# Optimization experiments

Measured on AMD Instinct MI355X. Metric: run time of the kernel, lower is better.

Reference implementation:

```python
import jax, jax.numpy as jnp
import numpy as np

B, S, H = 1, 2048, 4096
NH, NKV, D = 32, 8, 128
ROPE_THETA = 10000.0


def _rotate_half(x):
    half = x.shape[-1] // 2
    return jnp.concatenate([-x[..., half:], x[..., :half]], axis=-1)


def _rope_cos_sin(position_ids, dim, theta):
    inv_freq = 1.0 / (theta ** (jnp.arange(0, dim, 2, dtype=jnp.float32) / dim))  # [D/2]
    freqs = position_ids.astype(jnp.float32)[..., None] * inv_freq  # [B,S,D/2]
    emb = jnp.concatenate([freqs, freqs], axis=-1)  # [B,S,D]
    return jnp.cos(emb)[:, None], jnp.sin(emb)[:, None]  # [B,1,S,D]


def setup_inputs() -> dict:
    key = jax.random.key(0)
    k1, k2, k3 = jax.random.split(key, 3)
    hidden_states = jax.random.normal(k1, (B, S, H), dtype=jnp.float32)
    # fused QKV weight: columns = [NH*D | NKV*D | NKV*D]
    w_qkv = jax.random.normal(k2, (H, (NH + 2 * NKV) * D), dtype=jnp.float32) * (1.0 / np.sqrt(H))
    w_o = jax.random.normal(k3, (NH * D, H), dtype=jnp.float32) * (1.0 / np.sqrt(NH * D))
    attention_mask = jnp.tril(jnp.ones((S, S), dtype=bool))[None, None]  # causal [1,1,S,S]
    position_ids = jnp.arange(S, dtype=jnp.int64 if jax.config.jax_enable_x64 else jnp.int32)[None, :]
    return {"hidden_states": hidden_states, "w_qkv": w_qkv, "w_o": w_o,
            "attention_mask": attention_mask, "position_ids": position_ids}


def reference(hidden_states, w_qkv, w_o, attention_mask, position_ids):
    bsz, q_len, _ = hidden_states.shape
    qk_scale = 1.0 / np.sqrt(D)

    # fused QKV projection
    qkv = jnp.einsum('bsh,hc->bsc', hidden_states, w_qkv)
    q = qkv[..., : NH * D].reshape(bsz, q_len, NH, D).transpose(0, 2, 1, 3)        # [B,NH,S,D]
    k = qkv[..., NH * D: (NH + NKV) * D].reshape(bsz, q_len, NKV, D).transpose(0, 2, 1, 3)
    v = qkv[..., (NH + NKV) * D:].reshape(bsz, q_len, NKV, D).transpose(0, 2, 1, 3)

    # RoPE
    cos, sin = _rope_cos_sin(position_ids, D, ROPE_THETA)
    q = q * cos + _rotate_half(q) * sin
    k = k * cos + _rotate_half(k) * sin

    # GQA expand kv heads
    groups = NH // NKV
    k = jnp.repeat(k, groups, axis=1)  # [B,NH,S,D]
    v = jnp.repeat(v, groups, axis=1)

    # causal masked attention (eager path, matches scaled_qk + softmax(fp32))
    scores = jnp.einsum('bhqd,bhkd->bhqk', q, k) * qk_scale
    scores = jnp.where(attention_mask, scores, jnp.finfo(scores.dtype).min)
    probs = jax.nn.softmax(scores.astype(jnp.float32), axis=-1).astype(q.dtype)
    attn = jnp.einsum('bhqk,bhkd->bhqd', probs, v)  # [B,NH,S,D]

    # merge heads + output projection
    attn = attn.transpose(0, 2, 1, 3).reshape(bsz, q_len, NH * D)
    return jnp.einsum('bsd,dh->bsh', attn, w_o)
```

## Files before the change

### kernel.cpp

```cpp
#include <hip/hip_runtime.h>
#include <cstdint>
#include <cstddef>


#define DEV __device__ __forceinline__

typedef __attribute__((ext_vector_type(4))) float  f32x4;
typedef __attribute__((ext_vector_type(4))) short  short4v;
typedef __attribute__((ext_vector_type(8))) short  short8;
typedef __attribute__((ext_vector_type(8))) __bf16 bf16x8;

DEV short f32_to_bf16(float x) {
  union { float f; uint32_t u; } v; v.f = x;
  uint32_t r = v.u + 0x7fffu + ((v.u >> 16) & 1u);
  return (short)(r >> 16);
}

union frag_u { short4v h[2]; bf16x8 v; short s[8]; uint32_t u[4]; };
DEV bf16x8 comb(short4v lo, short4v hi) { frag_u u; u.h[0] = lo; u.h[1] = hi; return u.v; }

DEV uint32_t pack2bf_trunc(float a, float b) {
  union { float f; uint32_t u; } x, y; x.f = a; y.f = b;
  return (x.u >> 16) | (y.u & 0xFFFF0000u);
}

DEV f32x4 MFMA(bf16x8 a, bf16x8 b, f32x4 c) {
  return __builtin_amdgcn_mfma_f32_16x16x32_bf16(a, b, c, 0, 0, 0);
}

typedef __attribute__((address_space(1))) void* gas1p;
typedef __attribute__((address_space(3))) void* as3p;
DEV void gld16(const void* g, void* l) {
  __builtin_amdgcn_global_load_lds((gas1p)g, (as3p)l, 16, 0, 0);
}

#define VMCNT(n) asm volatile("s_waitcnt vmcnt(" #n ")" ::: "memory")


__global__ __launch_bounds__(256) void k_cvt_bf16(const float* __restrict__ x,
                                                  short* __restrict__ y, int n4) {
  int i = blockIdx.x * 256 + threadIdx.x;
  int stride = gridDim.x * 256;
  for (; i < n4; i += stride) {
    f32x4 v = ((const f32x4*)x)[i];
    short4v o;
    o[0] = f32_to_bf16(v[0]); o[1] = f32_to_bf16(v[1]);
    o[2] = f32_to_bf16(v[2]); o[3] = f32_to_bf16(v[3]);
    ((short4v*)y)[i] = o;
  }
}

__global__ __launch_bounds__(256) void k_transpose64(const float* __restrict__ src,
                                                     short* __restrict__ dst,
                                                     int R, int C, int stride) {
  __shared__ float tile[64][65];
  const int c0 = blockIdx.x * 64, r0 = blockIdx.y * 64;
  const int t = threadIdx.x;
  const int lr = t >> 4;
  const int lc = (t & 15) * 4;
  #pragma unroll
  for (int p = 0; p < 4; ++p) {
    const int r = p * 16 + lr;
    f32x4 v = *(const f32x4*)(src + (long)(r0 + r) * stride + c0 + lc);
    tile[r][lc] = v[0]; tile[r][lc + 1] = v[1]; tile[r][lc + 2] = v[2]; tile[r][lc + 3] = v[3];
  }
  __syncthreads();
  #pragma unroll
  for (int p = 0; p < 4; ++p) {
    const int c = p * 16 + lr;
    short4v o;
    o[0] = f32_to_bf16(tile[lc][c]);     o[1] = f32_to_bf16(tile[lc + 1][c]);
    o[2] = f32_to_bf16(tile[lc + 2][c]); o[3] = f32_to_bf16(tile[lc + 3][c]);
    *(short4v*)(dst + (long)(c0 + c) * R + r0 + lc) = o;
  }
}

__global__ __launch_bounds__(256) void k_vtrans64(const float* __restrict__ C1,
                                                  short* __restrict__ Vt) {
  __shared__ float tile[64][65];
  const int s0 = blockIdx.x * 64, d0 = blockIdx.y * 64, z = blockIdx.z;
  const int t = threadIdx.x;
  const int lr = t >> 4;
  const int lc = (t & 15) * 4;
  const float* src = C1 + 5120 + z * 128;
  #pragma unroll
  for (int p = 0; p < 4; ++p) {
    const int r = p * 16 + lr;
    f32x4 v = *(const f32x4*)(src + (long)(s0 + r) * 6144 + d0 + lc);
    tile[r][lc] = v[0]; tile[r][lc + 1] = v[1]; tile[r][lc + 2] = v[2]; tile[r][lc + 3] = v[3];
  }
  __syncthreads();
  short* dst = Vt + (long)z * 128 * 2048;
  #pragma unroll
  for (int p = 0; p < 4; ++p) {
    const int d = p * 16 + lr;
    short4v o;
    o[0] = f32_to_bf16(tile[lc][d]);     o[1] = f32_to_bf16(tile[lc + 1][d]);
    o[2] = f32_to_bf16(tile[lc + 2][d]); o[3] = f32_to_bf16(tile[lc + 3][d]);
    *(short4v*)(dst + (long)(d0 + d) * 2048 + s0 + lc) = o;
  }
}

__global__ __launch_bounds__(256) void k_rope_pack(const float* __restrict__ C1,
                                                   short* __restrict__ Qh,
                                                   short* __restrict__ Kh) {
  __shared__ float cs[64], sn[64];
  const int s = blockIdx.x, t = threadIdx.x;
  if (t < 64) {
    float inv = powf(10000.0f, -(float)t * (1.0f / 64.0f));
    float a = (float)s * inv;
    cs[t] = cosf(a);
    sn[t] = sinf(a);
  }
  __syncthreads();
  const float* row = C1 + (long)s * 6144;
  for (int i = t; i < 2048; i += 256) {
    int hh = i >> 6, j = i & 63;
    float c = cs[j], ss = sn[j];
    float x0 = row[hh * 128 + j], x1 = row[hh * 128 + j + 64];
    long o = ((long)hh * 2048 + s) * 128 + j;
    Qh[o]      = f32_to_bf16(x0 * c - x1 * ss);
    Qh[o + 64] = f32_to_bf16(x1 * c + x0 * ss);
  }
  for (int i = t; i < 512; i += 256) {
    int hh = i >> 6, j = i & 63;
    float c = cs[j], ss = sn[j];
    float x0 = row[4096 + hh * 128 + j], x1 = row[4096 + hh * 128 + j + 64];
    long o = ((long)hh * 2048 + s) * 128 + j;
    Kh[o]      = f32_to_bf16(x0 * c - x1 * ss);
    Kh[o + 64] = f32_to_bf16(x1 * c + x0 * ss);
  }
}


template<int MR>
DEV void gemm8p_engine(const short* __restrict__ A, const short* __restrict__ Bt,
                       float* __restrict__ Cp, int N, int K,
                       char* __restrict__ AsB, char* __restrict__ BsB) {
  constexpr int BM = MR * 32;
  const int tid = threadIdx.x;
  const int lane = tid & 63;
  const int w = tid >> 6;
  const int wm = w >> 2, wn = w & 3;
  const int wr = wm * (MR * 16);
  const int wc = wn * 64;
  const int g = lane >> 4, r16 = lane & 15;
  const long m0 = (long)blockIdx.y * BM;
  const long n0 = (long)blockIdx.x * 256;
  const int l8 = lane >> 3, l7 = lane & 7;
  const int sslot = l7 ^ l8;

  f32x4 acc[MR][4] = {};
  const int NT = K >> 6;

  auto stageA = [&](int h, int kt, int bufn) {
    #pragma unroll
    for (int s = 0; s < BM / 128; ++s) {
      const int rb = h * (BM / 2) + s * 64 + w * 8;
      gld16(A + (m0 + rb + l8) * (long)K + kt * 64 + sslot * 8,
            AsB + ((size_t)bufn * BM + rb) * 128);
    }
  };
  auto stageB = [&](int h, int kt, int bufn) {
    #pragma unroll
    for (int s = 0; s < 2; ++s) {
      const int rb = h * 128 + s * 64 + w * 8;
      gld16(Bt + (n0 + rb + l8) * (long)K + kt * 64 + sslot * 8,
            BsB + ((size_t)bufn * 256 + rb) * 128);
    }
  };

  bf16x8 a[MR / 2][2], b0[2][2], b1[2][2];

  #define LDA_HALF(h, buf) { _Pragma("unroll") for (int m = 0; m < MR/2; ++m) \
      _Pragma("unroll") for (int kk = 0; kk < 2; ++kk) { \
        const int row = wr + ((h) * (MR/2) + m) * 16 + r16; \
        const int slot = ((kk << 2) | g) ^ (r16 & 7); \
        a[m][kk] = *(const bf16x8*)(AsB + ((size_t)(buf) * BM + row) * 128 + slot * 16); } }
  #define LDB_HALF(dst, h, buf) { _Pragma("unroll") for (int n = 0; n < 2; ++n) \
      _Pragma("unroll") for (int kk = 0; kk < 2; ++kk) { \
        const int row = wc + ((h) * 2 + n) * 16 + r16; \
        const int slot = ((kk << 2) | g) ^ (r16 & 7); \
        dst[n][kk] = *(const bf16x8*)(BsB + ((size_t)(buf) * 256 + row) * 128 + slot * 16); } }
  #define QUADQ(mh, nh, bb) { __builtin_amdgcn_s_setprio(1); \
      _Pragma("unroll") for (int m = 0; m < MR/2; ++m) \
      _Pragma("unroll") for (int n = 0; n < 2; ++n) \
      _Pragma("unroll") for (int kk = 0; kk < 2; ++kk) \
        acc[(mh) * (MR/2) + m][(nh) * 2 + n] = \
          MFMA(a[m][kk], bb[n][kk], acc[(mh) * (MR/2) + m][(nh) * 2 + n]); \
      __builtin_amdgcn_s_setprio(0); }

  stageA(0, 0, 0); stageB(0, 0, 0); stageB(1, 0, 0); stageA(1, 0, 0);
  VMCNT(4);
  __builtin_amdgcn_s_barrier();

  for (int t = 0; t < NT - 1; ++t) {
    const int buf = t & 1, bufn = buf ^ 1, tn = t + 1;
    LDA_HALF(0, buf); LDB_HALF(b0, 0, buf);
    stageA(0, tn, bufn);
    __builtin_amdgcn_s_barrier();
    QUADQ(0, 0, b0);
    VMCNT(4);
    __builtin_amdgcn_s_barrier();
    LDB_HALF(b1, 1, buf);
    stageB(0, tn, bufn);
    __builtin_amdgcn_s_barrier();
    QUADQ(0, 1, b1);
    VMCNT(4);
    __builtin_amdgcn_s_barrier();
    LDA_HALF(1, buf);
    stageB(1, tn, bufn);
    __builtin_amdgcn_s_barrier();
    QUADQ(1, 1, b1);
    __builtin_amdgcn_s_barrier();
    stageA(1, tn, bufn);
    QUADQ(1, 0, b0);
    VMCNT(4);
    __builtin_amdgcn_s_barrier();
  }
  {
    const int buf = (NT - 1) & 1;
    LDA_HALF(0, buf); LDB_HALF(b0, 0, buf);
    __builtin_amdgcn_s_barrier();
    QUADQ(0, 0, b0);
    VMCNT(2);
    __builtin_amdgcn_s_barrier();
    LDB_HALF(b1, 1, buf);
    __builtin_amdgcn_s_barrier();
    QUADQ(0, 1, b1);
    VMCNT(0);
    __builtin_amdgcn_s_barrier();
    LDA_HALF(1, buf);
    __builtin_amdgcn_s_barrier();
    QUADQ(1, 1, b1);
    QUADQ(1, 0, b0);
  }
  #undef LDA_HALF
  #undef LDB_HALF
  #undef QUADQ

  #pragma unroll
  for (int m = 0; m < MR; ++m) {
    #pragma unroll
    for (int n = 0; n < 4; ++n) {
      const long col = n0 + wc + n * 16 + r16;
      #pragma unroll
      for (int j = 0; j < 4; ++j) {
        const long row = m0 + wr + m * 16 + g * 4 + j;
        Cp[row * N + col] = acc[m][n][j];
      }
    }
  }
}

__global__ __launch_bounds__(512, 2) void k_gemm1_8p(const short* __restrict__ A,
                                                     const short* __restrict__ Bt,
                                                     float* __restrict__ C, int N, int K) {
  __shared__ short As[2][256][64];
  __shared__ short Bs[2][256][64];
  gemm8p_engine<8>(A, Bt, C, N, K, (char*)&As[0][0][0], (char*)&Bs[0][0][0]);
}


template<int OUT_BF16>
__global__ __launch_bounds__(256, 2) void k_gemm128(const short* __restrict__ A,
                                                    const short* __restrict__ Bt,
                                                    void* __restrict__ Cp,
                                                    int M, int N, int K) {
  __shared__ short As[2][128][64];
  __shared__ short Bs[2][128][64];
  const int tid = threadIdx.x;
  const int lane = tid & 63;
  const int w = tid >> 6;
  const int wr = (w >> 1) * 64;
  const int wc = (w & 1) * 64;
  const int g = lane >> 4, r16 = lane & 15;
  const long m0 = (long)blockIdx.y * 128;
  const long n0 = (long)blockIdx.x * 128;
  const int l8 = lane >> 3, l7 = lane & 7;
  const int sslot = l7 ^ l8;

  f32x4 acc[4][4] = {};
  const int NT = K >> 6;

  auto stageTile = [&](int kt, int buf) {
    #pragma unroll
    for (int L = 0; L < 4; ++L) {
      const int rb = (w * 4 + L) * 8;
      gld16(A  + (m0 + rb + l8) * (long)K + kt * 64 + sslot * 8, (char*)&As[buf][rb][0]);
      gld16(Bt + (n0 + rb + l8) * (long)K + kt * 64 + sslot * 8, (char*)&Bs[buf][rb][0]);
    }
  };
  auto ldA = [&](int m, int kk, int buf) -> bf16x8 {
    const int row = wr + m * 16 + r16;
    const int slot = ((kk << 2) | g) ^ (r16 & 7);
    return *(const bf16x8*)((const char*)&As[buf][0][0] + row * 128 + slot * 16);
  };
  auto ldB = [&](int n, int kk, int buf) -> bf16x8 {
    const int row = wc + n * 16 + r16;
    const int slot = ((kk << 2) | g) ^ (r16 & 7);
    return *(const bf16x8*)((const char*)&Bs[buf][0][0] + row * 128 + slot * 16);
  };

  stageTile(0, 0);
  __syncthreads();

  for (int t = 0; t < NT; ++t) {
    const int buf = t & 1;
    if (t + 1 < NT) stageTile(t + 1, buf ^ 1);

    bf16x8 a[2][2], b[2][2];
    #pragma unroll
    for (int mh = 0; mh < 2; ++mh) {
      #pragma unroll
      for (int m = 0; m < 2; ++m)
        #pragma unroll
        for (int kk = 0; kk < 2; ++kk) a[m][kk] = ldA(mh * 2 + m, kk, buf);
      #pragma unroll
      for (int nh = 0; nh < 2; ++nh) {
        #pragma unroll
        for (int n = 0; n < 2; ++n)
          #pragma unroll
          for (int kk = 0; kk < 2; ++kk) b[n][kk] = ldB(nh * 2 + n, kk, buf);
        #pragma unroll
        for (int m = 0; m < 2; ++m)
          #pragma unroll
          for (int n = 0; n < 2; ++n)
            #pragma unroll
            for (int kk = 0; kk < 2; ++kk)
              acc[mh * 2 + m][nh * 2 + n] =
                MFMA(a[m][kk], b[n][kk], acc[mh * 2 + m][nh * 2 + n]);
      }
    }
    __syncthreads();
  }

  #pragma unroll
  for (int m = 0; m < 4; ++m) {
    #pragma unroll
    for (int n = 0; n < 4; ++n) {
      const long col = n0 + wc + n * 16 + r16;
      #pragma unroll
      for (int j = 0; j < 4; ++j) {
        const long row = m0 + wr + m * 16 + g * 4 + j;
        if (OUT_BF16) ((short*)Cp)[row * N + col] = f32_to_bf16(acc[m][n][j]);
        else          ((float*)Cp)[row * N + col] = acc[m][n][j];
      }
    }
  }
}


__global__ __launch_bounds__(256, 2) void k_attn(const short* __restrict__ Qh,
                                                 const short* __restrict__ Kh,
                                                 const short* __restrict__ Vt,
                                                 short* __restrict__ O) {
  __shared__ short Kl[64][136];
  __shared__ short Vl[128][72];
  const int h = blockIdx.x, by = blockIdx.y, hk = h >> 2;
  const int qt = (by < 8) ? (2 * by) : (15 - 2 * (by - 8));
  const int tid = threadIdx.x, lane = tid & 63, w = tid >> 6;
  const int g = lane >> 4, r16 = lane & 15;
  const int q0w = qt * 128 + w * 32;

  bf16x8 qf[2][4];
  #pragma unroll
  for (int qb = 0; qb < 2; ++qb) {
    const short* qb_ptr = Qh + ((long)h * 2048 + q0w + qb * 16 + r16) * 128;
    #pragma unroll
    for (int c = 0; c < 4; ++c) {
      short4v lo = *(const short4v*)(qb_ptr + 32 * c + 4 * g);
      short4v hi = *(const short4v*)(qb_ptr + 32 * c + 16 + 4 * g);
      qf[qb][c] = comb(lo, hi);
    }
  }
  const short* Kg = Kh + (long)hk * (2048 * 128);
  const short* Vg = Vt + (long)hk * (128 * 2048);

  f32x4 accO[2][8] = {};
  float mrun[2] = {-1e30f, -1e30f}, lrun[2] = {0.0f, 0.0f};
  const int NTB = 2 * qt + 2;

  short8 kpre[4], vpre[4];
  #pragma unroll
  for (int j = 0; j < 4; ++j) {
    const int n = tid + j * 256;
    kpre[j] = *(const short8*)(Kg + ((long)(n >> 4)) * 128 + (n & 15) * 8);
    vpre[j] = *(const short8*)(Vg + (long)(n >> 3) * 2048 + (n & 7) * 8);
  }

  for (int kt = 0; kt < NTB; ++kt) {
    #pragma unroll
    for (int j = 0; j < 4; ++j) {
      const int n = tid + j * 256;
      *(short8*)(&Kl[n >> 4][(n & 15) * 8]) = kpre[j];
      *(short8*)(&Vl[n >> 3][(n & 7) * 8]) = vpre[j];
    }
    __syncthreads();

    if (kt + 1 < NTB) {
      const long koff = (long)(kt + 1) * 64;
      #pragma unroll
      for (int j = 0; j < 4; ++j) {
        const int n = tid + j * 256;
        kpre[j] = *(const short8*)(Kg + (koff + (n >> 4)) * 128 + (n & 15) * 8);
        vpre[j] = *(const short8*)(Vg + (long)(n >> 3) * 2048 + koff + (n & 7) * 8);
      }
    }

    if (kt * 64 <= q0w + 31) {
      f32x4 accS[2][4] = {};
      __builtin_amdgcn_s_setprio(1);
      #pragma unroll
      for (int kvf = 0; kvf < 4; ++kvf) {
        const short* kr = &Kl[kvf * 16 + r16][0];
        #pragma unroll
        for (int c = 0; c < 4; ++c) {
          short4v lo = *(const short4v*)(kr + 32 * c + 4 * g);
          short4v hi = *(const short4v*)(kr + 32 * c + 16 + 4 * g);
          bf16x8 af = comb(lo, hi);
          accS[0][kvf] = MFMA(af, qf[0][c], accS[0][kvf]);
          accS[1][kvf] = MFMA(af, qf[1][c], accS[1][kvf]);
        }
      }
      __builtin_amdgcn_s_setprio(0);

      const bool diag = (kt * 64 + 63 > q0w);
      frag_u p0[2], p1[2];
      #pragma unroll
      for (int qb = 0; qb < 2; ++qb) {
        const int q_glob = q0w + qb * 16 + r16;
        float sc[4][4];
        #pragma unroll
        for (int kvf = 0; kvf < 4; ++kvf)
          #pragma unroll
          for (int r = 0; r < 4; ++r) sc[kvf][r] = accS[qb][kvf][r] * 0.08838834764831845f;
        if (diag) {
          #pragma unroll
          for (int kvf = 0; kvf < 4; ++kvf)
            #pragma unroll
            for (int r = 0; r < 4; ++r) {
              const int kvg = kt * 64 + kvf * 16 + g * 4 + r;
              if (kvg > q_glob) sc[kvf][r] = -1e30f;
            }
        }
        float rm[4];
        #pragma unroll
        for (int kvf = 0; kvf < 4; ++kvf)
          rm[kvf] = fmaxf(fmaxf(sc[kvf][0], sc[kvf][1]), fmaxf(sc[kvf][2], sc[kvf][3]));
        float mt = fmaxf(fmaxf(rm[0], rm[1]), fmaxf(rm[2], rm[3]));
        mt = fmaxf(mt, __shfl_xor(mt, 16));
        mt = fmaxf(mt, __shfl_xor(mt, 32));

        const bool nonew = __all(mt <= mrun[qb]);
        const float mnew = nonew ? mrun[qb] : fmaxf(mrun[qb], mt);
        float pk[4];
        #pragma unroll
        for (int kvf = 0; kvf < 4; ++kvf) {
          #pragma unroll
          for (int r = 0; r < 4; ++r) sc[kvf][r] = __expf(sc[kvf][r] - mnew);
          pk[kvf] = (sc[kvf][0] + sc[kvf][1]) + (sc[kvf][2] + sc[kvf][3]);
        }
        float ps = (pk[0] + pk[1]) + (pk[2] + pk[3]);
        ps += __shfl_xor(ps, 16);
        ps += __shfl_xor(ps, 32);
        if (nonew) {
          lrun[qb] += ps;
        } else {
          const float scale = __expf(mrun[qb] - mnew);
          lrun[qb] = lrun[qb] * scale + ps;
          mrun[qb] = mnew;
          #pragma unroll
          for (int df = 0; df < 8; ++df)
            #pragma unroll
            for (int j = 0; j < 4; ++j) accO[qb][df][j] *= scale;
        }
        p0[qb].u[0] = pack2bf_trunc(sc[0][0], sc[0][1]);
        p0[qb].u[1] = pack2bf_trunc(sc[0][2], sc[0][3]);
        p0[qb].u[2] = pack2bf_trunc(sc[1][0], sc[1][1]);
        p0[qb].u[3] = pack2bf_trunc(sc[1][2], sc[1][3]);
        p1[qb].u[0] = pack2bf_trunc(sc[2][0], sc[2][1]);
        p1[qb].u[1] = pack2bf_trunc(sc[2][2], sc[2][3]);
        p1[qb].u[2] = pack2bf_trunc(sc[3][0], sc[3][1]);
        p1[qb].u[3] = pack2bf_trunc(sc[3][2], sc[3][3]);
      }

      __builtin_amdgcn_s_setprio(1);
      #pragma unroll
      for (int df = 0; df < 8; ++df) {
        const short* vr = &Vl[df * 16 + r16][0];
        short4v a0 = *(const short4v*)(vr + 4 * g);
        short4v a1 = *(const short4v*)(vr + 16 + 4 * g);
        short4v a2 = *(const short4v*)(vr + 32 + 4 * g);
        short4v a3 = *(const short4v*)(vr + 48 + 4 * g);
        bf16x8 v01 = comb(a0, a1), v23 = comb(a2, a3);
        accO[0][df] = MFMA(v01, p0[0].v, accO[0][df]);
        accO[0][df] = MFMA(v23, p1[0].v, accO[0][df]);
        accO[1][df] = MFMA(v01, p0[1].v, accO[1][df]);
        accO[1][df] = MFMA(v23, p1[1].v, accO[1][df]);
      }
      __builtin_amdgcn_s_setprio(0);
    }
    __syncthreads();
  }

  #pragma unroll
  for (int qb = 0; qb < 2; ++qb) {
    const int q_glob = q0w + qb * 16 + r16;
    const float invl = 1.0f / lrun[qb];
    #pragma unroll
    for (int df = 0; df < 8; ++df) {
      const int d0 = df * 16 + g * 4;
      short4v o;
      #pragma unroll
      for (int j = 0; j < 4; ++j) o[j] = f32_to_bf16(accO[qb][df][j] * invl);
      *(short4v*)(O + (long)q_glob * 4096 + h * 128 + d0) = o;
    }
  }
}


extern "C" void kernel_launch(void* const* d_in, const int* in_sizes, int n_in,
                              void* d_out, int out_size, void* d_ws, size_t ws_size,
                              hipStream_t stream) {
  const float* hs   = (const float*)d_in[0];
  const float* wqkv = (const float*)d_in[1];
  const float* wo   = (const float*)d_in[2];

  const size_t OFF_HSB = 0;
  const size_t OFF_W1T = 16777216;
  const size_t OFF_WOT = 67108864;
  const size_t OFF_C1  = 100663296;
  const size_t OFF_KH  = 152043520;
  const size_t OFF_VT  = 156237824;
  if (ws_size < 160432128u) return;

  char* ws = (char*)d_ws;
  short* hsb = (short*)(ws + OFF_HSB);
  short* W1T = (short*)(ws + OFF_W1T);
  short* WoT = (short*)(ws + OFF_WOT);
  float* C1  = (float*)(ws + OFF_C1);
  short* Kh  = (short*)(ws + OFF_KH);
  short* Vt  = (short*)(ws + OFF_VT);
  short* Qh  = hsb;
  short* AO  = (short*)(ws + OFF_C1);

  k_cvt_bf16<<<2048, 256, 0, stream>>>(hs, hsb, 2048 * 4096 / 4);
  k_transpose64<<<dim3(96, 64), 256, 0, stream>>>(wqkv, W1T, 4096, 6144, 6144);
  k_transpose64<<<dim3(64, 64), 256, 0, stream>>>(wo, WoT, 4096, 4096, 4096);
  k_gemm1_8p<<<dim3(24, 8), 512, 0, stream>>>(hsb, W1T, C1, 6144, 4096);
  k_rope_pack<<<2048, 256, 0, stream>>>(C1, Qh, Kh);
  k_vtrans64<<<dim3(32, 2, 8), 256, 0, stream>>>(C1, Vt);
  k_attn<<<dim3(32, 16), 256, 0, stream>>>(Qh, Kh, Vt, AO);
  k_gemm128<0><<<dim3(32, 16), 256, 0, stream>>>(AO, WoT, (void*)d_out, 2048, 4096, 4096);
}
```

Before: 350.1 us.

## Double-buffer K/V shared tiles in attention kernel to drop a barrier per step

Shared memory tiles for K and V become double-buffered. The next tile is written into the alternate buffer midway through the current iteration, after the softmax and before the PV MFMAs, so only one __syncthreads per iteration remains. The aim is to overlap LDS stores with compute and cut barrier stalls. Shared memory use doubles to about 70KB per block, which may limit the 2-blocks-per-CU occupancy target.

```diff
diff --git a/kernel.cpp b/kernel.cpp
--- a/kernel.cpp
+++ b/kernel.cpp
@@ -355,8 +355,8 @@
                                                  const short* __restrict__ Kh,
                                                  const short* __restrict__ Vt,
                                                  short* __restrict__ O) {
-  __shared__ short Kl[64][136];
-  __shared__ short Vl[128][72];
+  __shared__ short Kl[2][64][136];
+  __shared__ short Vl[2][128][72];
   const int h = blockIdx.x, by = blockIdx.y, hk = h >> 2;
   const int qt = (by < 8) ? (2 * by) : (15 - 2 * (by - 8));
   const int tid = threadIdx.x, lane = tid & 63, w = tid >> 6;
@@ -388,17 +388,18 @@
     kpre[j] = *(const short8*)(Kg + ((long)(n >> 4)) * 128 + (n & 15) * 8);
     vpre[j] = *(const short8*)(Vg + (long)(n >> 3) * 2048 + (n & 7) * 8);
   }
+  #pragma unroll
+  for (int j = 0; j < 4; ++j) {
+    const int n = tid + j * 256;
+    *(short8*)(&Kl[0][n >> 4][(n & 15) * 8]) = kpre[j];
+    *(short8*)(&Vl[0][n >> 3][(n & 7) * 8]) = vpre[j];
+  }
+  __syncthreads();
 
   for (int kt = 0; kt < NTB; ++kt) {
-    #pragma unroll
-    for (int j = 0; j < 4; ++j) {
-      const int n = tid + j * 256;
-      *(short8*)(&Kl[n >> 4][(n & 15) * 8]) = kpre[j];
-      *(short8*)(&Vl[n >> 3][(n & 7) * 8]) = vpre[j];
-    }
-    __syncthreads();
-
-    if (kt + 1 < NTB) {
+    const int cb = kt & 1;
+    const bool more = (kt + 1 < NTB);
+    if (more) {
       const long koff = (long)(kt + 1) * 64;
       #pragma unroll
       for (int j = 0; j < 4; ++j) {
@@ -408,12 +409,13 @@
       }
     }
 
-    if (kt * 64 <= q0w + 31) {
-      f32x4 accS[2][4] = {};
+    const bool active = (kt * 64 <= q0w + 31);
+    f32x4 accS[2][4] = {};
+    if (active) {
       __builtin_amdgcn_s_setprio(1);
       #pragma unroll
       for (int kvf = 0; kvf < 4; ++kvf) {
-        const short* kr = &Kl[kvf * 16 + r16][0];
+        const short* kr = &Kl[cb][kvf * 16 + r16][0];
         #pragma unroll
         for (int c = 0; c < 4; ++c) {
           short4v lo = *(const short4v*)(kr + 32 * c + 4 * g);
@@ -424,9 +426,11 @@
         }
       }
       __builtin_amdgcn_s_setprio(0);
-
+    }
+
+    frag_u p0[2], p1[2];
+    if (active) {
       const bool diag = (kt * 64 + 63 > q0w);
-      frag_u p0[2], p1[2];
       #pragma unroll
       for (int qb = 0; qb < 2; ++qb) {
         const int q_glob = q0w + qb * 16 + r16;
@@ -484,11 +488,22 @@
         p1[qb].u[2] = pack2bf_trunc(sc[3][0], sc[3][1]);
         p1[qb].u[3] = pack2bf_trunc(sc[3][2], sc[3][3]);
       }
-
+    }
+
+    if (more) {
+      #pragma unroll
+      for (int j = 0; j < 4; ++j) {
+        const int n = tid + j * 256;
+        *(short8*)(&Kl[cb ^ 1][n >> 4][(n & 15) * 8]) = kpre[j];
+        *(short8*)(&Vl[cb ^ 1][n >> 3][(n & 7) * 8]) = vpre[j];
+      }
+    }
+
+    if (active) {
       __builtin_amdgcn_s_setprio(1);
       #pragma unroll
       for (int df = 0; df < 8; ++df) {
-        const short* vr = &Vl[df * 16 + r16][0];
+        const short* vr = &Vl[cb][df * 16 + r16][0];
         short4v a0 = *(const short4v*)(vr + 4 * g);
         short4v a1 = *(const short4v*)(vr + 16 + 4 * g);
         short4v a2 = *(const short4v*)(vr + 32 + 4 * g);
```

Result: slower. 392.7 us (+12.2%).
